# Performance work log

Measured on AMD Instinct MI355X. Metric: run time of the kernel, lower is better.

The kernel has to match this reference:

```python
import jax, jax.numpy as jnp
import numpy as np


def setup_inputs() -> dict:
    key = jax.random.key(0)
    k1, k2, k3, k4 = jax.random.split(key, 4)
    H, D, Dh, NH = 4096, 1024, 256, 4  # height, weight1, INNER_FEATURE_A, heads
    x = jax.random.normal(k1, (H, D), dtype=jnp.float32)
    Wq = jax.random.normal(k2, (NH, D, Dh), dtype=jnp.float32)
    lin_w = jax.random.normal(k3, (D, NH * Dh), dtype=jnp.float32)  # torch Linear weight [out, in]
    lin_b = jax.random.normal(k4, (D,), dtype=jnp.float32)
    return {"x": x, "Wq": Wq, "lin_w": lin_w, "lin_b": lin_b}


def reference(x, Wq, lin_w, lin_b):
    # Faithful to source: Q = K = V = x @ Wq1 (original uses Wq1 for all three).
    # mask_flag=False -> multiplicative all-ones mask (identity, elided).
    # qkv: [heads, H, Dh]
    qkv = jnp.einsum('hd,ndk->nhk', x, Wq)
    # scores: [heads, H, H]; softmax over dim=1 of the 2D matrix = last axis here
    scores = jnp.einsum('nqk,npk->nqp', qkv, qkv)
    attn = jax.nn.softmax(scores, axis=-1)
    z = jnp.einsum('nqp,npk->nqk', attn, qkv)  # [heads, H, Dh]
    # concat heads along feature dim -> [H, heads*Dh]
    zc = jnp.transpose(z, (1, 0, 2)).reshape(x.shape[0], -1)
    return zc @ lin_w.T + lin_b
```

## Files before the change

### kernel.cpp

```cpp
#include <hip/hip_runtime.h>
#include <math.h>

#define SEQ 4096
#define DIM 1024
#define DHEAD 256
#define NHEADS 4

typedef __attribute__((ext_vector_type(8))) short bf16x8;
typedef __attribute__((ext_vector_type(4))) float f32x4;
typedef __attribute__((ext_vector_type(4))) short short4v;
typedef __attribute__((ext_vector_type(8))) short short8v;

__device__ __forceinline__ unsigned short f2b(float f) {
    union { float f; unsigned u; } v; v.f = f;
    unsigned r = v.u + 0x7FFFu + ((v.u >> 16) & 1u);
    return (unsigned short)(r >> 16);
}
__device__ __forceinline__ float b2f(unsigned short u) {
    union { unsigned u; float f; } v; v.u = ((unsigned)u) << 16;
    return v.f;
}

__device__ __forceinline__ void gll16(const void* g, void* lds) {
    __builtin_amdgcn_global_load_lds(
        (const __attribute__((address_space(1))) unsigned*)g,
        (__attribute__((address_space(3))) unsigned*)lds, 16, 0, 0);
}

__device__ __forceinline__ f32x4 mfma16(bf16x8 a, bf16x8 b, f32x4 c) {
    return __builtin_amdgcn_mfma_f32_16x16x32_bf16(a, b, c, 0, 0, 0);
}

__global__ __launch_bounds__(256)
void conv_kernel(const float* __restrict__ in, unsigned short* __restrict__ out, int n4) {
    int i = blockIdx.x * 256 + threadIdx.x;
    if (i >= n4) return;
    float4 v = ((const float4*)in)[i];
    short4v o;
    o[0] = (short)f2b(v.x); o[1] = (short)f2b(v.y);
    o[2] = (short)f2b(v.z); o[3] = (short)f2b(v.w);
    *(short4v*)(out + (size_t)i * 4) = o;
}

__global__ __launch_bounds__(256)
void wqt_kernel(const float* __restrict__ Wq, unsigned short* __restrict__ WqT) {
    __shared__ unsigned short T[64][72];
    const int tid = threadIdx.x;
    const int h = blockIdx.z;
    const int d0 = blockIdx.x * 64, c0 = blockIdx.y * 64;
#pragma unroll
    for (int it = 0; it < 4; ++it) {
        int f = tid + 256 * it;
        int row = f >> 4, cg = f & 15;
        float4 v = *(const float4*)&Wq[((size_t)(h * DIM + d0 + row)) * DHEAD + c0 + cg * 4];
        T[row][cg * 4 + 0] = f2b(v.x); T[row][cg * 4 + 1] = f2b(v.y);
        T[row][cg * 4 + 2] = f2b(v.z); T[row][cg * 4 + 3] = f2b(v.w);
    }
    __syncthreads();
#pragma unroll
    for (int it = 0; it < 2; ++it) {
        int f = tid + 256 * it;
        int cl = f >> 3, dg = f & 7;
        short8v o;
#pragma unroll
        for (int e = 0; e < 8; ++e) o[e] = (short)T[dg * 8 + e][cl];
        *(short8v*)&WqT[((size_t)(h * DHEAD + c0 + cl)) * DIM + d0 + dg * 8] = o;
    }
}

__global__ __launch_bounds__(256)
void qkvt_kernel(const unsigned short* __restrict__ qkv, unsigned short* __restrict__ qkvT) {
    __shared__ unsigned short T[64][72];
    const int tid = threadIdx.x;
    const int h = blockIdx.z;
    const int r0 = blockIdx.x * 64, c0 = blockIdx.y * 64;
#pragma unroll
    for (int it = 0; it < 2; ++it) {
        int f = tid + 256 * it;
        int row = f >> 3, cg = f & 7;
        short8v v = *(const short8v*)&qkv[((size_t)h * SEQ + r0 + row) * DHEAD + c0 + cg * 8];
#pragma unroll
        for (int e = 0; e < 8; ++e) T[row][cg * 8 + e] = (unsigned short)v[e];
    }
    __syncthreads();
#pragma unroll
    for (int it = 0; it < 2; ++it) {
        int f = tid + 256 * it;
        int cl = f >> 3, rg = f & 7;
        short8v o;
#pragma unroll
        for (int e = 0; e < 8; ++e) o[e] = (short)T[rg * 8 + e][cl];
        *(short8v*)&qkvT[((size_t)h * DHEAD + c0 + cl) * SEQ + r0 + rg * 8] = o;
    }
}

__global__ __launch_bounds__(256)
void qkv_gemm_kernel(const unsigned short* __restrict__ A,
                     const unsigned short* __restrict__ B,
                     unsigned short* __restrict__ qkv) {
    __shared__ unsigned short As[128 * 64];
    __shared__ unsigned short Bs[128 * 64];
    const int tid = threadIdx.x, w = tid >> 6, l = tid & 63;
    const int g = l >> 4, r16 = l & 15;
    const int m0 = blockIdx.x * 128, n0 = blockIdx.y * 128;
    const int wm = (w >> 1) * 64, wn = (w & 1) * 64;

    f32x4 acc[4][4];
#pragma unroll
    for (int mr = 0; mr < 4; ++mr)
#pragma unroll
        for (int nr = 0; nr < 4; ++nr) acc[mr][nr] = (f32x4){0.f, 0.f, 0.f, 0.f};

    for (int kb = 0; kb < DIM; kb += 64) {
        __syncthreads();
#pragma unroll
        for (int cc = 0; cc < 4; ++cc) {
            int row = w * 32 + cc * 8 + (l >> 3);
            int c = (l & 7) ^ (row & 7);
            gll16(&A[(size_t)(m0 + row) * DIM + kb + c * 8], &As[(size_t)(w * 32 + cc * 8) * 64]);
            gll16(&B[(size_t)(n0 + row) * DIM + kb + c * 8], &Bs[(size_t)(w * 32 + cc * 8) * 64]);
        }
        __syncthreads();
#pragma unroll
        for (int s = 0; s < 2; ++s) {
            bf16x8 af[4], bf[4];
#pragma unroll
            for (int mr = 0; mr < 4; ++mr) {
                int row = wm + mr * 16 + r16;
                int st = (s * 4 + g) ^ (row & 7);
                af[mr] = *(const bf16x8*)&As[row * 64 + st * 8];
            }
#pragma unroll
            for (int nr = 0; nr < 4; ++nr) {
                int row = wn + nr * 16 + r16;
                int st = (s * 4 + g) ^ (row & 7);
                bf[nr] = *(const bf16x8*)&Bs[row * 64 + st * 8];
            }
#pragma unroll
            for (int mr = 0; mr < 4; ++mr)
#pragma unroll
                for (int nr = 0; nr < 4; ++nr)
                    acc[mr][nr] = mfma16(af[mr], bf[nr], acc[mr][nr]);
        }
    }
#pragma unroll
    for (int mr = 0; mr < 4; ++mr)
#pragma unroll
        for (int nr = 0; nr < 4; ++nr) {
            int n = n0 + wn + nr * 16 + r16;
            int h = n >> 8, c = n & 255;
#pragma unroll
            for (int r = 0; r < 4; ++r) {
                int m = m0 + wm + mr * 16 + g * 4 + r;
                qkv[((size_t)h * SEQ + m) * DHEAD + c] = f2b(acc[mr][nr][r]);
            }
        }
}

__global__ __launch_bounds__(512, 2)
void attn_kernel(const unsigned short* __restrict__ qkv,
                 const unsigned short* __restrict__ qkvT,
                 unsigned short* __restrict__ p0,
                 unsigned short* __restrict__ p1,
                 float* __restrict__ ml) {
    __shared__ unsigned short Ks[2][64 * 256];
    __shared__ unsigned short Vt[2][256 * 64];
    __shared__ unsigned short Ps[8][16 * 64];

    const int tid = threadIdx.x, w = tid >> 6, l = tid & 63;
    const int g = l >> 4, r16 = l & 15;
    const int bid = blockIdx.x;
    const int h = (bid & 7) >> 1, hf = bid & 1;
    const int qb = bid >> 3;
    const unsigned short* __restrict__ qh = qkv + (size_t)h * SEQ * DHEAD;
    const unsigned short* __restrict__ qth = qkvT + (size_t)h * DHEAD * SEQ;
    const int jb0 = hf * (SEQ / 2);
    const int NT = (SEQ / 2) / 64;

    bf16x8 qf[8];
    {
        const unsigned short* qrow =
            qh + (size_t)(qb * 128 + w * 16 + r16) * DHEAD + g * 8;
#pragma unroll
        for (int s = 0; s < 8; ++s) qf[s] = *(const bf16x8*)(qrow + s * 32);
    }

#define STAGEK(buf, jb)                                                             \
    {                                                                               \
        _Pragma("unroll")                                                           \
        for (int cc = 0; cc < 4; ++cc) {                                            \
            int ch = w * 4 + cc;                          \
            int j = ch * 2 + (l >> 5);                                              \
            int cp = l & 31;                                                        \
            int c = (cp & 24) | ((cp & 7) ^ (j & 7));                               \
            gll16(&qh[(size_t)((jb) + j) * DHEAD + c * 8], &Ks[buf][(size_t)ch * 512]); \
        }                                                                           \
    }
#define STAGEV(buf, jb)                                                             \
    {                                                                               \
        _Pragma("unroll")                                                           \
        for (int cc = 0; cc < 4; ++cc) {                                            \
            int ch = w * 4 + cc;                         \
            int d = ch * 8 + (l >> 3);                                              \
            int c = (l & 7) ^ (d & 7);                                              \
            gll16(&qth[(size_t)d * SEQ + (jb) + c * 8], &Vt[buf][(size_t)ch * 512]); \
        }                                                                           \
    }

    STAGEK(0, jb0); STAGEV(0, jb0);
    STAGEK(1, jb0 + 64); STAGEV(1, jb0 + 64);

    f32x4 Oacc[16];
#pragma unroll
    for (int i = 0; i < 16; ++i) Oacc[i] = (f32x4){0.f, 0.f, 0.f, 0.f};
    float mrow = -INFINITY, lrow = 0.f;

    for (int t = 0; t < NT; ++t) {
        const int cur = t & 1;

        __builtin_amdgcn_sched_barrier(0);
        if (t + 1 < NT) { asm volatile("s_waitcnt vmcnt(8)" ::: "memory"); }
        else            { asm volatile("s_waitcnt vmcnt(0)" ::: "memory"); }
        __builtin_amdgcn_s_barrier();
        __builtin_amdgcn_sched_barrier(0);

        const unsigned short* Kb = &Ks[cur][0];
        f32x4 sacc[4];
#pragma unroll
        for (int jt = 0; jt < 4; ++jt) sacc[jt] = (f32x4){0.f, 0.f, 0.f, 0.f};
        __builtin_amdgcn_s_setprio(1);
#pragma unroll
        for (int s = 0; s < 8; ++s)
#pragma unroll
            for (int jt = 0; jt < 4; ++jt) {
                int j = jt * 16 + r16;
                int c = s * 4 + g;
                int st = (c & 24) | ((c & 7) ^ (j & 7));
                bf16x8 af = *(const bf16x8*)&Kb[j * 256 + st * 8];
                sacc[jt] = mfma16(af, qf[s], sacc[jt]);
            }
        __builtin_amdgcn_s_setprio(0);

        float mx = sacc[0][0];
#pragma unroll
        for (int jt = 0; jt < 4; ++jt)
#pragma unroll
            for (int r = 0; r < 4; ++r) mx = fmaxf(mx, sacc[jt][r]);
        mx = fmaxf(mx, __shfl_xor(mx, 16, 64));
        mx = fmaxf(mx, __shfl_xor(mx, 32, 64));

        const bool needr = !__all(mx <= mrow + 8.f);
        float alpha = 1.f;
        if (needr) {
            float mn = fmaxf(mrow, mx);
            alpha = __expf(mrow - mn);
            mrow = mn;
        }

        float rsum = 0.f;
        short4v pf[4];
#pragma unroll
        for (int jt = 0; jt < 4; ++jt)
#pragma unroll
            for (int r = 0; r < 4; ++r) {
                float p = __expf(sacc[jt][r] - mrow);
                rsum += p;
                pf[jt][r] = (short)f2b(p);
            }
        rsum += __shfl_xor(rsum, 16, 64);
        rsum += __shfl_xor(rsum, 32, 64);
        lrow = lrow * alpha + rsum;

#pragma unroll
        for (int jt = 0; jt < 4; ++jt) {
            int st = (2 * jt + (g >> 1)) ^ (r16 & 7);
            *(short4v*)&Ps[w][r16 * 64 + st * 8 + (g & 1) * 4] = pf[jt];
        }

        if (needr) {
            float av[4];
#pragma unroll
            for (int r = 0; r < 4; ++r) av[r] = __shfl(alpha, 4 * g + r, 64);
#pragma unroll
            for (int dt = 0; dt < 16; ++dt)
#pragma unroll
                for (int r = 0; r < 4; ++r) Oacc[dt][r] *= av[r];
        }

        asm volatile("s_waitcnt lgkmcnt(0)" ::: "memory");
        __builtin_amdgcn_sched_barrier(0);

        bf16x8 pa[2];
#pragma unroll
        for (int s2 = 0; s2 < 2; ++s2) {
            int st = (4 * s2 + g) ^ (r16 & 7);
            pa[s2] = *(const bf16x8*)&Ps[w][r16 * 64 + st * 8];
        }

        const unsigned short* Vb = &Vt[cur][0];
        __builtin_amdgcn_s_setprio(1);
#pragma unroll
        for (int dt = 0; dt < 16; ++dt) {
            int d = dt * 16 + r16;
#pragma unroll
            for (int s2 = 0; s2 < 2; ++s2) {
                int st = (4 * s2 + g) ^ (d & 7);
                bf16x8 bv = *(const bf16x8*)&Vb[d * 64 + st * 8];
                Oacc[dt] = mfma16(pa[s2], bv, Oacc[dt]);
            }
        }
        __builtin_amdgcn_s_setprio(0);

        __builtin_amdgcn_sched_barrier(0);
        __builtin_amdgcn_s_barrier();
        __builtin_amdgcn_sched_barrier(0);
        if (t + 2 < NT) {
            const int jb2 = jb0 + (t + 2) * 64;
            STAGEK(cur, jb2); STAGEV(cur, jb2);
        }
        __builtin_amdgcn_sched_barrier(0);
    }
#undef STAGEK
#undef STAGEV

    unsigned short* po = hf ? p1 : p0;
#pragma unroll
    for (int dt = 0; dt < 16; ++dt) {
        int d = dt * 16 + r16;
#pragma unroll
        for (int r = 0; r < 4; ++r) {
            int q = qb * 128 + w * 16 + 4 * g + r;
            po[(size_t)q * (NHEADS * DHEAD) + h * DHEAD + d] = f2b(Oacc[dt][r]);
        }
    }
    if (g == 0) {
        int q = qb * 128 + w * 16 + r16;
        float* mlq = ml + ((size_t)(hf * NHEADS + h) * SEQ + q) * 2;
        mlq[0] = mrow; mlq[1] = lrow;
    }
}

__global__ __launch_bounds__(256)
void combine_kernel(const unsigned short* __restrict__ pa,
                    const unsigned short* __restrict__ pb,
                    const float* __restrict__ ml,
                    unsigned short* __restrict__ zc) {
    size_t t = (size_t)blockIdx.x * 256 + threadIdx.x;
    size_t f = t * 8;
    int q = (int)(f >> 10);
    int h = (int)((f >> 8) & 3);
    const float* ml0 = ml + ((size_t)h * SEQ + q) * 2;
    const float* ml1 = ml + ((size_t)(NHEADS + h) * SEQ + q) * 2;
    float m0 = ml0[0], l0 = ml0[1], m1 = ml1[0], l1 = ml1[1];
    float M = fmaxf(m0, m1);
    float e0 = __expf(m0 - M), e1 = __expf(m1 - M);
    float inv = 1.f / (e0 * l0 + e1 * l1);
    e0 *= inv; e1 *= inv;
    short8v a = *(const short8v*)(pa + f);
    short8v b = *(const short8v*)(pb + f);
    short8v o;
#pragma unroll
    for (int e = 0; e < 8; ++e)
        o[e] = (short)f2b(e0 * b2f((unsigned short)a[e]) + e1 * b2f((unsigned short)b[e]));
    *(short8v*)(zc + f) = o;
}

__global__ __launch_bounds__(256)
void out_gemm_kernel(const unsigned short* __restrict__ A,
                     const unsigned short* __restrict__ B,
                     const float* __restrict__ lb, float* __restrict__ out) {
    __shared__ unsigned short As[128 * 64];
    __shared__ unsigned short Bs[128 * 64];
    const int tid = threadIdx.x, w = tid >> 6, l = tid & 63;
    const int g = l >> 4, r16 = l & 15;
    const int m0 = blockIdx.x * 128, n0 = blockIdx.y * 128;
    const int wm = (w >> 1) * 64, wn = (w & 1) * 64;

    f32x4 acc[4][4];
#pragma unroll
    for (int mr = 0; mr < 4; ++mr)
#pragma unroll
        for (int nr = 0; nr < 4; ++nr) acc[mr][nr] = (f32x4){0.f, 0.f, 0.f, 0.f};

    for (int kb = 0; kb < DIM; kb += 64) {
        __syncthreads();
#pragma unroll
        for (int cc = 0; cc < 4; ++cc) {
            int row = w * 32 + cc * 8 + (l >> 3);
            int c = (l & 7) ^ (row & 7);
            gll16(&A[(size_t)(m0 + row) * DIM + kb + c * 8], &As[(size_t)(w * 32 + cc * 8) * 64]);
            gll16(&B[(size_t)(n0 + row) * DIM + kb + c * 8], &Bs[(size_t)(w * 32 + cc * 8) * 64]);
        }
        __syncthreads();
#pragma unroll
        for (int s = 0; s < 2; ++s) {
            bf16x8 af[4], bf[4];
#pragma unroll
            for (int mr = 0; mr < 4; ++mr) {
                int row = wm + mr * 16 + r16;
                int st = (s * 4 + g) ^ (row & 7);
                af[mr] = *(const bf16x8*)&As[row * 64 + st * 8];
            }
#pragma unroll
            for (int nr = 0; nr < 4; ++nr) {
                int row = wn + nr * 16 + r16;
                int st = (s * 4 + g) ^ (row & 7);
                bf[nr] = *(const bf16x8*)&Bs[row * 64 + st * 8];
            }
#pragma unroll
            for (int mr = 0; mr < 4; ++mr)
#pragma unroll
                for (int nr = 0; nr < 4; ++nr)
                    acc[mr][nr] = mfma16(af[mr], bf[nr], acc[mr][nr]);
        }
    }
#pragma unroll
    for (int mr = 0; mr < 4; ++mr)
#pragma unroll
        for (int nr = 0; nr < 4; ++nr) {
            int n = n0 + wn + nr * 16 + r16;
            float bv = lb[n];
#pragma unroll
            for (int r = 0; r < 4; ++r) {
                int m = m0 + wm + mr * 16 + g * 4 + r;
                out[(size_t)m * DIM + n] = acc[mr][nr][r] + bv;
            }
        }
}

extern "C" void kernel_launch(void* const* d_in, const int* in_sizes, int n_in,
                              void* d_out, int out_size, void* d_ws, size_t ws_size,
                              hipStream_t stream) {
    const float* x  = (const float*)d_in[0];
    const float* Wq = (const float*)d_in[1];
    const float* lw = (const float*)d_in[2];
    const float* lb = (const float*)d_in[3];
    float* out = (float*)d_out;

    char* wsb = (char*)d_ws;
    unsigned short* qkvb = (unsigned short*)(wsb);
    unsigned short* qkvT = (unsigned short*)(wsb + ((size_t)8 << 20));
    unsigned short* xb   = (unsigned short*)(wsb + ((size_t)16 << 20));
    unsigned short* p0   = xb;
    unsigned short* WqT  = (unsigned short*)(wsb + ((size_t)24 << 20));
    float*          ml   = (float*)(wsb + ((size_t)24 << 20));
    unsigned short* lwb  = (unsigned short*)(wsb + ((size_t)26 << 20));
    unsigned short* p1   = (unsigned short*)d_out;

    conv_kernel<<<4096, 256, 0, stream>>>(x, xb, (SEQ * DIM) / 4);
    conv_kernel<<<1024, 256, 0, stream>>>(lw, lwb, (DIM * DIM) / 4);
    wqt_kernel<<<dim3(16, 4, 4), 256, 0, stream>>>(Wq, WqT);
    qkv_gemm_kernel<<<dim3(SEQ / 128, DIM / 128), 256, 0, stream>>>(xb, WqT, qkvb);
    qkvt_kernel<<<dim3(64, 4, 4), 256, 0, stream>>>(qkvb, qkvT);
    attn_kernel<<<256, 512, 0, stream>>>(qkvb, qkvT, p0, p1, ml);
    combine_kernel<<<(SEQ * DIM / 8) / 256, 256, 0, stream>>>(p0, p1, ml, p0);
    out_gemm_kernel<<<dim3(SEQ / 128, DIM / 128), 256, 0, stream>>>(p0, lwb, lb, out);
}
```

Baseline: 167.9 us.

## Use 32x32 MFMA attention with register-shuffled P and three-way KV split

The attention kernel moves from 16x16x32 to 32x32x16 bf16 MFMAs, with 256 query rows per block and 32-key tiles. The softmax probabilities are repacked through cross-lane shuffles instead of an LDS round trip. The key range is split unevenly into three chunks (44/42/42 tiles), giving 192 blocks instead of 256 two-way-split blocks, and the combine kernel merges three partials. The aim is higher MFMA efficiency, less LDS traffic, and better wave balance across CUs. In exchange, the kernel uses more registers for the Q fragments and accumulators, and the workspace aliasing moves qkvT and a partial buffer into the output buffer.

```diff
diff --git a/kernel.cpp b/kernel.cpp
--- a/kernel.cpp
+++ b/kernel.cpp
@@ -8,6 +8,7 @@
 
 typedef __attribute__((ext_vector_type(8))) short bf16x8;
 typedef __attribute__((ext_vector_type(4))) float f32x4;
+typedef __attribute__((ext_vector_type(16))) float f32x16;
 typedef __attribute__((ext_vector_type(4))) short short4v;
 typedef __attribute__((ext_vector_type(8))) short short8v;
 
@@ -29,6 +30,9 @@
 
 __device__ __forceinline__ f32x4 mfma16(bf16x8 a, bf16x8 b, f32x4 c) {
     return __builtin_amdgcn_mfma_f32_16x16x32_bf16(a, b, c, 0, 0, 0);
+}
+__device__ __forceinline__ f32x16 mfma32(bf16x8 a, bf16x8 b, f32x16 c) {
+    return __builtin_amdgcn_mfma_f32_32x32x16_bf16(a, b, c, 0, 0, 0);
 }
 
 __global__ __launch_bounds__(256)
@@ -162,151 +166,132 @@
                  const unsigned short* __restrict__ qkvT,
                  unsigned short* __restrict__ p0,
                  unsigned short* __restrict__ p1,
+                 unsigned short* __restrict__ p2,
                  float* __restrict__ ml) {
-    __shared__ unsigned short Ks[2][64 * 256];
-    __shared__ unsigned short Vt[2][256 * 64];
-    __shared__ unsigned short Ps[8][16 * 64];
+    __shared__ unsigned short Ks[2][32 * 256];
+    __shared__ unsigned short Vt[2][256 * 32];
 
     const int tid = threadIdx.x, w = tid >> 6, l = tid & 63;
-    const int g = l >> 4, r16 = l & 15;
+    const int l31 = l & 31, hi = l >> 5;
     const int bid = blockIdx.x;
-    const int h = (bid & 7) >> 1, hf = bid & 1;
-    const int qb = bid >> 3;
+    const int qb = bid / 12, rem = bid % 12;
+    const int h = rem / 3, tt = rem % 3;
+    const int jb0 = (tt == 0) ? 0 : 1408 + (tt - 1) * 1344;
+    const int NT = (tt == 0) ? 44 : 42;
     const unsigned short* __restrict__ qh = qkv + (size_t)h * SEQ * DHEAD;
     const unsigned short* __restrict__ qth = qkvT + (size_t)h * DHEAD * SEQ;
-    const int jb0 = hf * (SEQ / 2);
-    const int NT = (SEQ / 2) / 64;
-
-    bf16x8 qf[8];
-    {
-        const unsigned short* qrow =
-            qh + (size_t)(qb * 128 + w * 16 + r16) * DHEAD + g * 8;
-#pragma unroll
-        for (int s = 0; s < 8; ++s) qf[s] = *(const bf16x8*)(qrow + s * 32);
-    }
-
-#define STAGEK(buf, jb)                                                             \
+
+    const int qrow = qb * 256 + w * 32 + l31;
+    bf16x8 qf[16];
+#pragma unroll
+    for (int s = 0; s < 16; ++s)
+        qf[s] = *(const bf16x8*)&qh[(size_t)qrow * DHEAD + s * 16 + hi * 8];
+
+#define STAGE(buf, jb)                                                              \
     {                                                                               \
         _Pragma("unroll")                                                           \
-        for (int cc = 0; cc < 4; ++cc) {                                            \
-            int ch = w * 4 + cc;                          \
+        for (int cc = 0; cc < 2; ++cc) {                                            \
+            int ch = w * 2 + cc;                          \
             int j = ch * 2 + (l >> 5);                                              \
             int cp = l & 31;                                                        \
             int c = (cp & 24) | ((cp & 7) ^ (j & 7));                               \
             gll16(&qh[(size_t)((jb) + j) * DHEAD + c * 8], &Ks[buf][(size_t)ch * 512]); \
         }                                                                           \
-    }
-#define STAGEV(buf, jb)                                                             \
-    {                                                                               \
         _Pragma("unroll")                                                           \
-        for (int cc = 0; cc < 4; ++cc) {                                            \
-            int ch = w * 4 + cc;                         \
-            int d = ch * 8 + (l >> 3);                                              \
-            int c = (l & 7) ^ (d & 7);                                              \
+        for (int cc = 0; cc < 2; ++cc) {                                            \
+            int ch = w * 2 + cc;                        \
+            int d = ch * 16 + (l >> 2);                                             \
+            int c = (l & 3) ^ (d & 3);                                              \
             gll16(&qth[(size_t)d * SEQ + (jb) + c * 8], &Vt[buf][(size_t)ch * 512]); \
         }                                                                           \
     }
 
-    STAGEK(0, jb0); STAGEV(0, jb0);
-    STAGEK(1, jb0 + 64); STAGEV(1, jb0 + 64);
-
-    f32x4 Oacc[16];
-#pragma unroll
-    for (int i = 0; i < 16; ++i) Oacc[i] = (f32x4){0.f, 0.f, 0.f, 0.f};
+    STAGE(0, jb0);
+    STAGE(1, jb0 + 32);
+
+    f32x16 Oacc[8];
+#pragma unroll
+    for (int i = 0; i < 8; ++i) Oacc[i] = (f32x16)(0.f);
     float mrow = -INFINITY, lrow = 0.f;
 
     for (int t = 0; t < NT; ++t) {
         const int cur = t & 1;
 
         __builtin_amdgcn_sched_barrier(0);
-        if (t + 1 < NT) { asm volatile("s_waitcnt vmcnt(8)" ::: "memory"); }
+        if (t < NT - 1) { asm volatile("s_waitcnt vmcnt(4)" ::: "memory"); }
         else            { asm volatile("s_waitcnt vmcnt(0)" ::: "memory"); }
         __builtin_amdgcn_s_barrier();
         __builtin_amdgcn_sched_barrier(0);
 
         const unsigned short* Kb = &Ks[cur][0];
-        f32x4 sacc[4];
-#pragma unroll
-        for (int jt = 0; jt < 4; ++jt) sacc[jt] = (f32x4){0.f, 0.f, 0.f, 0.f};
+        f32x16 sacc = (f32x16)(0.f);
         __builtin_amdgcn_s_setprio(1);
 #pragma unroll
-        for (int s = 0; s < 8; ++s)
-#pragma unroll
-            for (int jt = 0; jt < 4; ++jt) {
-                int j = jt * 16 + r16;
-                int c = s * 4 + g;
-                int st = (c & 24) | ((c & 7) ^ (j & 7));
-                bf16x8 af = *(const bf16x8*)&Kb[j * 256 + st * 8];
-                sacc[jt] = mfma16(af, qf[s], sacc[jt]);
-            }
+        for (int s = 0; s < 16; ++s) {
+            int c = s * 2 + hi;
+            int st = (c & 24) | ((c & 7) ^ (l31 & 7));
+            bf16x8 kf = *(const bf16x8*)&Kb[l31 * 256 + st * 8];
+            sacc = mfma32(kf, qf[s], sacc);
+        }
         __builtin_amdgcn_s_setprio(0);
 
-        float mx = sacc[0][0];
-#pragma unroll
-        for (int jt = 0; jt < 4; ++jt)
-#pragma unroll
-            for (int r = 0; r < 4; ++r) mx = fmaxf(mx, sacc[jt][r]);
-        mx = fmaxf(mx, __shfl_xor(mx, 16, 64));
+        float mx = sacc[0];
+#pragma unroll
+        for (int r = 1; r < 16; ++r) mx = fmaxf(mx, sacc[r]);
         mx = fmaxf(mx, __shfl_xor(mx, 32, 64));
 
         const bool needr = !__all(mx <= mrow + 8.f);
-        float alpha = 1.f;
         if (needr) {
             float mn = fmaxf(mrow, mx);
-            alpha = __expf(mrow - mn);
+            float alpha = __expf(mrow - mn);
             mrow = mn;
+            lrow *= alpha;
+#pragma unroll
+            for (int dt = 0; dt < 8; ++dt) Oacc[dt] *= alpha;
         }
 
         float rsum = 0.f;
-        short4v pf[4];
-#pragma unroll
-        for (int jt = 0; jt < 4; ++jt)
-#pragma unroll
-            for (int r = 0; r < 4; ++r) {
-                float p = __expf(sacc[jt][r] - mrow);
-                rsum += p;
-                pf[jt][r] = (short)f2b(p);
-            }
-        rsum += __shfl_xor(rsum, 16, 64);
+#pragma unroll
+        for (int r = 0; r < 16; ++r) {
+            float p = __expf(sacc[r] - mrow);
+            rsum += p;
+            sacc[r] = p;
+        }
         rsum += __shfl_xor(rsum, 32, 64);
-        lrow = lrow * alpha + rsum;
-
-#pragma unroll
-        for (int jt = 0; jt < 4; ++jt) {
-            int st = (2 * jt + (g >> 1)) ^ (r16 & 7);
-            *(short4v*)&Ps[w][r16 * 64 + st * 8 + (g & 1) * 4] = pf[jt];
-        }
-
-        if (needr) {
-            float av[4];
-#pragma unroll
-            for (int r = 0; r < 4; ++r) av[r] = __shfl(alpha, 4 * g + r, 64);
-#pragma unroll
-            for (int dt = 0; dt < 16; ++dt)
-#pragma unroll
-                for (int r = 0; r < 4; ++r) Oacc[dt][r] *= av[r];
-        }
-
-        asm volatile("s_waitcnt lgkmcnt(0)" ::: "memory");
-        __builtin_amdgcn_sched_barrier(0);
-
-        bf16x8 pa[2];
-#pragma unroll
-        for (int s2 = 0; s2 < 2; ++s2) {
-            int st = (4 * s2 + g) ^ (r16 & 7);
-            pa[s2] = *(const bf16x8*)&Ps[w][r16 * 64 + st * 8];
+        lrow += rsum;
+
+        unsigned pk8[8];
+#pragma unroll
+        for (int m = 0; m < 8; ++m)
+            pk8[m] = (unsigned)f2b(sacc[2 * m]) | ((unsigned)f2b(sacc[2 * m + 1]) << 16);
+        bf16x8 pbf[2];
+#pragma unroll
+        for (int js = 0; js < 2; ++js) {
+            unsigned a0 = pk8[js * 4 + 0], a1 = pk8[js * 4 + 1];
+            unsigned b0 = pk8[js * 4 + 2], b1 = pk8[js * 4 + 3];
+            unsigned sa0 = (unsigned)__shfl_xor((int)a0, 32, 64);
+            unsigned sa1 = (unsigned)__shfl_xor((int)a1, 32, 64);
+            unsigned sb0 = (unsigned)__shfl_xor((int)b0, 32, 64);
+            unsigned sb1 = (unsigned)__shfl_xor((int)b1, 32, 64);
+            union { unsigned u[4]; bf16x8 v; } U;
+            U.u[0] = hi ? sb0 : a0;
+            U.u[1] = hi ? sb1 : a1;
+            U.u[2] = hi ? b0 : sa0;
+            U.u[3] = hi ? b1 : sa1;
+            pbf[js] = U.v;
         }
 
         const unsigned short* Vb = &Vt[cur][0];
         __builtin_amdgcn_s_setprio(1);
 #pragma unroll
-        for (int dt = 0; dt < 16; ++dt) {
-            int d = dt * 16 + r16;
-#pragma unroll
-            for (int s2 = 0; s2 < 2; ++s2) {
-                int st = (4 * s2 + g) ^ (d & 7);
-                bf16x8 bv = *(const bf16x8*)&Vb[d * 64 + st * 8];
-                Oacc[dt] = mfma16(pa[s2], bv, Oacc[dt]);
+        for (int dt = 0; dt < 8; ++dt) {
+            int d = dt * 32 + l31;
+#pragma unroll
+            for (int js = 0; js < 2; ++js) {
+                int c = js * 2 + hi;
+                int st = c ^ (d & 3);
+                bf16x8 vf = *(const bf16x8*)&Vb[d * 32 + st * 8];
+                Oacc[dt] = mfma32(vf, pbf[js], Oacc[dt]);
             }
         }
         __builtin_amdgcn_s_setprio(0);
@@ -314,28 +299,24 @@
         __builtin_amdgcn_sched_barrier(0);
         __builtin_amdgcn_s_barrier();
         __builtin_amdgcn_sched_barrier(0);
-        if (t + 2 < NT) {
-            const int jb2 = jb0 + (t + 2) * 64;
-            STAGEK(cur, jb2); STAGEV(cur, jb2);
-        }
+        if (t + 2 < NT) STAGE(cur, jb0 + (t + 2) * 32);
         __builtin_amdgcn_sched_barrier(0);
     }
-#undef STAGEK
-#undef STAGEV
-
-    unsigned short* po = hf ? p1 : p0;
-#pragma unroll
-    for (int dt = 0; dt < 16; ++dt) {
-        int d = dt * 16 + r16;
-#pragma unroll
-        for (int r = 0; r < 4; ++r) {
-            int q = qb * 128 + w * 16 + 4 * g + r;
-            po[(size_t)q * (NHEADS * DHEAD) + h * DHEAD + d] = f2b(Oacc[dt][r]);
-        }
-    }
-    if (g == 0) {
-        int q = qb * 128 + w * 16 + r16;
-        float* mlq = ml + ((size_t)(hf * NHEADS + h) * SEQ + q) * 2;
+#undef STAGE
+
+    unsigned short* po = (tt == 0) ? p0 : (tt == 1) ? p1 : p2;
+#pragma unroll
+    for (int dt = 0; dt < 8; ++dt)
+#pragma unroll
+        for (int k = 0; k < 4; ++k) {
+            int d = dt * 32 + k * 8 + hi * 4;
+            short4v o;
+#pragma unroll
+            for (int i = 0; i < 4; ++i) o[i] = (short)f2b(Oacc[dt][4 * k + i]);
+            *(short4v*)&po[(size_t)qrow * (NHEADS * DHEAD) + h * DHEAD + d] = o;
+        }
+    if (hi == 0) {
+        float* mlq = ml + ((size_t)(tt * NHEADS + h) * SEQ + qrow) * 2;
         mlq[0] = mrow; mlq[1] = lrow;
     }
 }
@@ -343,25 +324,32 @@
 __global__ __launch_bounds__(256)
 void combine_kernel(const unsigned short* __restrict__ pa,
                     const unsigned short* __restrict__ pb,
+                    const unsigned short* __restrict__ pc,
                     const float* __restrict__ ml,
                     unsigned short* __restrict__ zc) {
     size_t t = (size_t)blockIdx.x * 256 + threadIdx.x;
     size_t f = t * 8;
     int q = (int)(f >> 10);
     int h = (int)((f >> 8) & 3);
-    const float* ml0 = ml + ((size_t)h * SEQ + q) * 2;
-    const float* ml1 = ml + ((size_t)(NHEADS + h) * SEQ + q) * 2;
-    float m0 = ml0[0], l0 = ml0[1], m1 = ml1[0], l1 = ml1[1];
-    float M = fmaxf(m0, m1);
-    float e0 = __expf(m0 - M), e1 = __expf(m1 - M);
-    float inv = 1.f / (e0 * l0 + e1 * l1);
-    e0 *= inv; e1 *= inv;
+    const float* ml0 = ml + ((size_t)(0 * NHEADS + h) * SEQ + q) * 2;
+    const float* ml1 = ml + ((size_t)(1 * NHEADS + h) * SEQ + q) * 2;
+    const float* ml2 = ml + ((size_t)(2 * NHEADS + h) * SEQ + q) * 2;
+    float m0 = ml0[0], l0 = ml0[1];
+    float m1 = ml1[0], l1 = ml1[1];
+    float m2 = ml2[0], l2 = ml2[1];
+    float M = fmaxf(fmaxf(m0, m1), m2);
+    float e0 = __expf(m0 - M), e1 = __expf(m1 - M), e2 = __expf(m2 - M);
+    float inv = 1.f / (e0 * l0 + e1 * l1 + e2 * l2);
+    e0 *= inv; e1 *= inv; e2 *= inv;
     short8v a = *(const short8v*)(pa + f);
     short8v b = *(const short8v*)(pb + f);
+    short8v c = *(const short8v*)(pc + f);
     short8v o;
 #pragma unroll
     for (int e = 0; e < 8; ++e)
-        o[e] = (short)f2b(e0 * b2f((unsigned short)a[e]) + e1 * b2f((unsigned short)b[e]));
+        o[e] = (short)f2b(e0 * b2f((unsigned short)a[e]) +
+                          e1 * b2f((unsigned short)b[e]) +
+                          e2 * b2f((unsigned short)c[e]));
     *(short8v*)(zc + f) = o;
 }
 
@@ -439,20 +427,21 @@
 
     char* wsb = (char*)d_ws;
     unsigned short* qkvb = (unsigned short*)(wsb);
-    unsigned short* qkvT = (unsigned short*)(wsb + ((size_t)8 << 20));
+    unsigned short* p0   = (unsigned short*)(wsb + ((size_t)8 << 20));
     unsigned short* xb   = (unsigned short*)(wsb + ((size_t)16 << 20));
-    unsigned short* p0   = xb;
+    unsigned short* p1   = xb;
     unsigned short* WqT  = (unsigned short*)(wsb + ((size_t)24 << 20));
     float*          ml   = (float*)(wsb + ((size_t)24 << 20));
     unsigned short* lwb  = (unsigned short*)(wsb + ((size_t)26 << 20));
-    unsigned short* p1   = (unsigned short*)d_out;
+    unsigned short* qkvT = (unsigned short*)d_out;
+    unsigned short* p2   = (unsigned short*)d_out + ((size_t)4 << 20);
 
     conv_kernel<<<4096, 256, 0, stream>>>(x, xb, (SEQ * DIM) / 4);
     conv_kernel<<<1024, 256, 0, stream>>>(lw, lwb, (DIM * DIM) / 4);
     wqt_kernel<<<dim3(16, 4, 4), 256, 0, stream>>>(Wq, WqT);
     qkv_gemm_kernel<<<dim3(SEQ / 128, DIM / 128), 256, 0, stream>>>(xb, WqT, qkvb);
     qkvt_kernel<<<dim3(64, 4, 4), 256, 0, stream>>>(qkvb, qkvT);
-    attn_kernel<<<256, 512, 0, stream>>>(qkvb, qkvT, p0, p1, ml);
-    combine_kernel<<<(SEQ * DIM / 8) / 256, 256, 0, stream>>>(p0, p1, ml, p0);
+    attn_kernel<<<192, 512, 0, stream>>>(qkvb, qkvT, p0, p1, p2, ml);
+    combine_kernel<<<(SEQ * DIM / 8) / 256, 256, 0, stream>>>(p0, p1, p2, ml, p0);
     out_gemm_kernel<<<dim3(SEQ / 128, DIM / 128), 256, 0, stream>>>(p0, lwb, lb, out);
 }
```

New measurement: 188.5 us. 1.12x slower.
